# Optimization experiments

Measured on AMD Instinct MI355X. Metric: run time of the kernel, lower is better.

Reference implementation:

```python
import jax, jax.numpy as jnp
import numpy as np

N = 240000
B = 2
GRID = (480, 360, 32)
NUM_CLASS = 20
IGNORE_LABEL = 0
MINB = np.array([0.0, -np.pi, -4.0], np.float32)
MAXB = np.array([50.0, np.pi, 2.0], np.float32)
EPS = 1e-5


def setup_inputs() -> dict:
    key = jax.random.key(0)
    ks = jax.random.split(key, 32)
    d = {}
    d['pt_fea'] = jax.random.normal(ks[0], (N, 6), jnp.float32)
    # cylindrical coords (rho, phi, z) uniformly inside the volume
    u = jax.random.uniform(ks[1], (N, 3), jnp.float32)
    d['xyz'] = u * jnp.asarray(MAXB - MINB) + jnp.asarray(MINB)
    d['batch_idx'] = jnp.sort(jax.random.randint(ks[2], (N,), 0, B)).astype(jnp.int64)
    d['pt_lab'] = jax.random.randint(ks[3], (N,), 0, NUM_CLASS).astype(jnp.int64)
    d['shuffled_ind'] = jnp.arange(N, dtype=jnp.int64)  # identity perm (deterministic)
    i = 4
    for name, c in [('bn0', 9), ('bn1', 64), ('bn2', 128), ('bn3', 256)]:
        d[name + '_g'] = jax.random.uniform(ks[i], (c,), jnp.float32, 0.5, 1.5); i += 1
        d[name + '_b'] = jax.random.normal(ks[i], (c,), jnp.float32) * 0.1; i += 1
        d[name + '_m'] = jax.random.normal(ks[i], (c,), jnp.float32) * 0.1; i += 1
        d[name + '_v'] = jax.random.uniform(ks[i], (c,), jnp.float32, 0.5, 1.5); i += 1
    for name, (fi, fo) in [('1', (9, 64)), ('2', (64, 128)), ('3', (128, 256)), ('4', (256, 256))]:
        d['w' + name] = jax.random.normal(ks[i], (fi, fo), jnp.float32) / np.sqrt(fi); i += 1
        d['b' + name] = jax.random.normal(ks[i], (fo,), jnp.float32) * 0.01; i += 1
    d['wc'] = jax.random.normal(ks[i], (256, 16), jnp.float32) / 16.0; i += 1
    d['bc'] = jax.random.normal(ks[i], (16,), jnp.float32) * 0.01
    return d


def _bn(x, g, b, m, v):
    return (x - m) * (g * jax.lax.rsqrt(v + EPS)) + b


def _ppmodel(feat, bn0_g, bn0_b, bn0_m, bn0_v, w1, b1, bn1_g, bn1_b, bn1_m, bn1_v,
             w2, b2, bn2_g, bn2_b, bn2_m, bn2_v, w3, b3, bn3_g, bn3_b, bn3_m, bn3_v, w4, b4):
    x = _bn(feat, bn0_g, bn0_b, bn0_m, bn0_v)
    x = jax.nn.relu(_bn(x @ w1 + b1, bn1_g, bn1_b, bn1_m, bn1_v))
    x = jax.nn.relu(_bn(x @ w2 + b2, bn2_g, bn2_b, bn2_m, bn2_v))
    x = jax.nn.relu(_bn(x @ w3 + b3, bn3_g, bn3_b, bn3_m, bn3_v))
    return x @ w4 + b4  # [N, 256]


def reference(pt_fea, xyz, batch_idx, pt_lab, shuffled_ind,
              bn0_g, bn0_b, bn0_m, bn0_v, w1, b1, bn1_g, bn1_b, bn1_m, bn1_v,
              w2, b2, bn2_g, bn2_b, bn2_m, bn2_v, w3, b3, bn3_g, bn3_b, bn3_m, bn3_v,
              w4, b4, wc, bc):
    minb = jnp.asarray(MINB)
    maxb = jnp.asarray(MAXB)
    grid = jnp.asarray(np.array(GRID, np.float32))
    intervals = (maxb - minb) / (grid - 1.0)

    clamped = jnp.clip(xyz, minb, maxb)
    ind = jnp.floor((clamped - minb) / intervals).astype(jnp.int32)  # [N,3]
    voxel_centers = (ind.astype(jnp.float32) + 0.5) * intervals + minb
    rel_xyz = xyz - voxel_centers
    feat = jnp.concatenate([rel_xyz, pt_fea], axis=1)  # [N,9]

    bi = batch_idx.astype(jnp.int32)
    counts = jnp.full((B,) + GRID + (NUM_CLASS,), IGNORE_LABEL, jnp.int32)
    counts = counts.at[bi, ind[:, 0], ind[:, 1], ind[:, 2], pt_lab].add(1)
    voxel_labels = jnp.argmax(counts, axis=-1).astype(jnp.int32)  # [B,480,360,32]

    feat = feat[shuffled_ind]

    flat = ((bi.astype(jnp.int64) * GRID[0] + ind[:, 0]) * GRID[1] + ind[:, 1]) * GRID[2] + ind[:, 2]
    unq, unq_inv = jnp.unique(flat, size=N, fill_value=-1, return_inverse=True)
    unq_inv = unq_inv.reshape(-1)

    processed = _ppmodel(feat, bn0_g, bn0_b, bn0_m, bn0_v, w1, b1, bn1_g, bn1_b, bn1_m, bn1_v,
                         w2, b2, bn2_g, bn2_b, bn2_m, bn2_v, w3, b3, bn3_g, bn3_b, bn3_m, bn3_v, w4, b4)
    pooled = jax.ops.segment_max(processed, unq_inv, num_segments=N)
    seg_cnt = jax.ops.segment_sum(jnp.ones((N,), jnp.float32), unq_inv, num_segments=N)
    pooled = jnp.where(seg_cnt[:, None] > 0, pooled, 0.0)  # zero out empty (padded) segments

    processed_pooled = jax.nn.relu(pooled @ wc + bc)  # fea_compression

    cat_pt_ind = jnp.concatenate([batch_idx[:, None], ind.astype(jnp.int64)], axis=1)
    return (unq, processed_pooled, voxel_labels, cat_pt_ind)
```

## Files before the change

kernel.cpp:

```cpp
#include <hip/hip_runtime.h>
#include <stdint.h>

#define N_PTS 240000
#define NV    11059200
#define NWORDS 172800
#define NB_PT 938
#define NB_WORD 675
#define NBLK_MLP 3750
#define PA 264

typedef __bf16 bf16x8 __attribute__((ext_vector_type(8)));
typedef short  short8 __attribute__((ext_vector_type(8)));
typedef float  f32x4  __attribute__((ext_vector_type(4)));

__device__ __forceinline__ unsigned short f2bf(float f) {
  unsigned u = __builtin_bit_cast(unsigned, f);
  return (unsigned short)((u + 0x7FFFu + ((u >> 16) & 1u)) >> 16);
}
__device__ __forceinline__ float bf2f(unsigned short h) {
  unsigned u = ((unsigned)h) << 16;
  return __builtin_bit_cast(float, u);
}

__device__ __forceinline__ unsigned block_sum(unsigned v, unsigned* s4, int t) {
  #pragma unroll
  for (int o = 32; o; o >>= 1) v += __shfl_down(v, o);
  if ((t & 63) == 0) s4[t >> 6] = v;
  __syncthreads();
  unsigned r = s4[0] + s4[1] + s4[2] + s4[3];
  __syncthreads();
  return r;
}

__global__ void prep_vox_kernel(
    const float* __restrict__ bng0, const float* __restrict__ bnb0, const float* __restrict__ bnm0, const float* __restrict__ bnv0,
    const float* __restrict__ bng1, const float* __restrict__ bnb1, const float* __restrict__ bnm1, const float* __restrict__ bnv1,
    const float* __restrict__ bng2, const float* __restrict__ bnb2, const float* __restrict__ bnm2, const float* __restrict__ bnv2,
    const float* __restrict__ bng3, const float* __restrict__ bnb3, const float* __restrict__ bnm3, const float* __restrict__ bnv3,
    const float* __restrict__ w1, const float* __restrict__ b1,
    const float* __restrict__ w2, const float* __restrict__ b2,
    const float* __restrict__ w3, const float* __restrict__ b3,
    const float* __restrict__ w4, const float* __restrict__ wc,
    float* __restrict__ s0, float* __restrict__ t0, float* __restrict__ w1e, float* __restrict__ be1,
    float* __restrict__ be2, float* __restrict__ be3,
    unsigned short* __restrict__ w2t, unsigned short* __restrict__ w3t, unsigned short* __restrict__ w4t,
    unsigned short* __restrict__ wct,
    const float* __restrict__ xyz, const int* __restrict__ bidx,
    unsigned* __restrict__ flatkeys, unsigned long long* __restrict__ bitmap,
    float* __restrict__ out_cat, float* __restrict__ out_unq)
{
  if (blockIdx.x < 256) {
    const int id = blockIdx.x * 256 + threadIdx.x;
    { int c = id >> 8, k = id & 255; w4t[c * 256 + k] = f2bf(w4[k * 256 + c]); }
    if (id < 32768) { int c = id >> 7, k = id & 127;
      float s = bng3[c] * rsqrtf(bnv3[c] + 1e-5f);
      w3t[c * 128 + k] = f2bf(w3[k * 256 + c] * s); }
    if (id < 8192) { int c = id >> 6, k = id & 63;
      float s = bng2[c] * rsqrtf(bnv2[c] + 1e-5f);
      w2t[c * 64 + k] = f2bf(w2[k * 128 + c] * s); }
    if (id < 4096) { int c = id >> 8, k = id & 255;
      wct[c * 256 + k] = f2bf(wc[k * 16 + c]); }
    if (id < 576) { int k = id / 64, c = id % 64;
      float s = bng1[c] * rsqrtf(bnv1[c] + 1e-5f);
      w1e[k * 64 + c] = w1[k * 64 + c] * s; }
    if (id < 64)  { float s = bng1[id] * rsqrtf(bnv1[id] + 1e-5f); be1[id] = (b1[id] - bnm1[id]) * s + bnb1[id]; }
    if (id < 128) { float s = bng2[id] * rsqrtf(bnv2[id] + 1e-5f); be2[id] = (b2[id] - bnm2[id]) * s + bnb2[id]; }
    if (id < 256) { float s = bng3[id] * rsqrtf(bnv3[id] + 1e-5f); be3[id] = (b3[id] - bnm3[id]) * s + bnb3[id]; }
    if (id < 9)   { float s = bng0[id] * rsqrtf(bnv0[id] + 1e-5f); s0[id] = s; t0[id] = bnb0[id] - bnm0[id] * s; }
    return;
  }
  const int j = (blockIdx.x - 256) * 256 + threadIdx.x;
  if (j >= N_PTS) return;
  out_unq[j] = -1.0f;
  const float PI_F = 3.14159265358979323846f;
  const float minb[3] = {0.0f, -PI_F, -4.0f};
  const float maxb[3] = {50.0f, PI_F, 2.0f};
  const float gm1[3]  = {479.0f, 359.0f, 31.0f};
  int ind[3];
  #pragma unroll
  for (int d = 0; d < 3; ++d) {
    float itv = (maxb[d] - minb[d]) / gm1[d];
    float x  = xyz[(size_t)j * 3 + d];
    float cl = fminf(fmaxf(x, minb[d]), maxb[d]);
    ind[d] = (int)floorf((cl - minb[d]) / itv);
  }
  const int bi = bidx[j];
  const unsigned flat = ((unsigned)(bi * 480 + ind[0]) * 360u + (unsigned)ind[1]) * 32u + (unsigned)ind[2];
  flatkeys[j] = flat;
  atomicOr(&bitmap[flat >> 6], 1ull << (flat & 63u));
  float* oc = out_cat + (size_t)j * 4;
  oc[0] = (float)bi; oc[1] = (float)ind[0]; oc[2] = (float)ind[1]; oc[3] = (float)ind[2];
}

__global__ void reduce_words(const unsigned long long* __restrict__ bm, unsigned* __restrict__ bsums) {
  __shared__ unsigned sh[256];
  const int w = blockIdx.x * 256 + threadIdx.x;
  sh[threadIdx.x] = (unsigned)__popcll(bm[w]);
  __syncthreads();
  for (int s = 128; s > 0; s >>= 1) { if (threadIdx.x < s) sh[threadIdx.x] += sh[threadIdx.x + s]; __syncthreads(); }
  if (threadIdx.x == 0) bsums[blockIdx.x] = sh[0];
}

__global__ __launch_bounds__(256) void scatter_unq(
    const unsigned long long* __restrict__ bm, const unsigned* __restrict__ bsums,
    unsigned* __restrict__ wordpref, unsigned* __restrict__ unqvals, float* __restrict__ out_unq)
{
  __shared__ unsigned sh[256];
  __shared__ unsigned s4[4];
  const int t = threadIdx.x, b = blockIdx.x;
  const int w = b * 256 + t;
  unsigned long long word = bm[w];
  unsigned own = (unsigned)__popcll(word);
  sh[t] = own; __syncthreads();
  for (int off = 1; off < 256; off <<= 1) {
    unsigned v = (t >= off) ? sh[t - off] : 0u;
    __syncthreads(); sh[t] += v; __syncthreads();
  }
  unsigned v = 0;
  for (int i = t; i < b; i += 256) v += bsums[i];
  const unsigned excl = block_sum(v, s4, t);
  unsigned r = excl + sh[t] - own;
  wordpref[w] = r;
  while (word) {
    int bit = __builtin_ctzll(word);
    unsigned id = (unsigned)w * 64u + (unsigned)bit;
    unqvals[r] = id;
    out_unq[r] = (float)id;
    ++r;
    word &= word - 1;
  }
}

__global__ void inv_kernel(const unsigned* __restrict__ flatkeys, const unsigned long long* __restrict__ bm,
                           const unsigned* __restrict__ wordpref,
                           unsigned* __restrict__ unq_inv, unsigned* __restrict__ cnt) {
  const int j = blockIdx.x * 256 + threadIdx.x;
  if (j >= N_PTS) return;
  const unsigned f = flatkeys[j];
  const unsigned w = f >> 6, b = f & 63u;
  const unsigned r = wordpref[w] + (unsigned)__popcll(bm[w] & ((1ull << b) - 1ull));
  unq_inv[j] = r;
  atomicAdd(&cnt[r], 1u);
}

__global__ void reduce_cnt(const unsigned* __restrict__ cnt, unsigned* __restrict__ bsums) {
  __shared__ unsigned sh[256];
  const int j = blockIdx.x * 256 + threadIdx.x;
  sh[threadIdx.x] = (j < N_PTS) ? cnt[j] : 0u;
  __syncthreads();
  for (int s = 128; s > 0; s >>= 1) { if (threadIdx.x < s) sh[threadIdx.x] += sh[threadIdx.x + s]; __syncthreads(); }
  if (threadIdx.x == 0) bsums[blockIdx.x] = sh[0];
}

__global__ __launch_bounds__(256) void scan_cnt(
    const unsigned* __restrict__ cnt, const unsigned* __restrict__ bsums,
    unsigned* __restrict__ off, unsigned* __restrict__ cur)
{
  __shared__ unsigned sh[256];
  __shared__ unsigned s4[4];
  const int t = threadIdx.x, b = blockIdx.x;
  const int j = b * 256 + t;
  unsigned own = (j < N_PTS) ? cnt[j] : 0u;
  sh[t] = own; __syncthreads();
  for (int o = 1; o < 256; o <<= 1) {
    unsigned v = (t >= o) ? sh[t - o] : 0u;
    __syncthreads(); sh[t] += v; __syncthreads();
  }
  unsigned v = 0;
  for (int i = t; i < b; i += 256) v += bsums[i];
  const unsigned excl = block_sum(v, s4, t);
  if (j < N_PTS) { unsigned e = excl + sh[t] - own; off[j] = e; cur[j] = e; }
}

__global__ void plist_fill_kernel(const unsigned* __restrict__ unq_inv, unsigned* __restrict__ cur,
                                  unsigned long long* __restrict__ plist64,
                                  const unsigned* __restrict__ cnt, const float* __restrict__ bc,
                                  float* __restrict__ out_pooled) {
  const int j = blockIdx.x * 256 + threadIdx.x;
  if (j >= N_PTS) return;
  const unsigned r = unq_inv[j];
  plist64[atomicAdd(&cur[r], 1u)] = ((unsigned long long)r << 32) | (unsigned)j;
  if (cnt[j] == 0) {
    #pragma unroll
    for (int c = 0; c < 16; ++c) out_pooled[(size_t)j * 16 + c] = fmaxf(bc[c], 0.f);
  }
}

template<int K, int C, bool RELU, bool MIDB>
__device__ __forceinline__ void gemm_stage(
    const unsigned short* __restrict__ Wt,
    const float* __restrict__ bias,
    const unsigned short* in,
    unsigned short* outp,
    int wave, int l15, int quad)
{
  constexpr int KC = K / 32;
  constexpr int NT = C / 64;
  f32x4 acc[4][NT];
  #pragma unroll
  for (int mt = 0; mt < 4; ++mt)
    #pragma unroll
    for (int nt = 0; nt < NT; ++nt) acc[mt][nt] = (f32x4){0.f, 0.f, 0.f, 0.f};
  const unsigned short* wp[NT];
  #pragma unroll
  for (int nt = 0; nt < NT; ++nt)
    wp[nt] = Wt + (size_t)(wave * 16 * NT + nt * 16 + l15) * K + quad * 8;
  bf16x8 b0[NT], b1r[NT], b2r[NT];
  #pragma unroll
  for (int nt = 0; nt < NT; ++nt)
    b0[nt] = __builtin_bit_cast(bf16x8, *(const short8*)(wp[nt]));
  if (KC > 1) {
    #pragma unroll
    for (int nt = 0; nt < NT; ++nt)
      b1r[nt] = __builtin_bit_cast(bf16x8, *(const short8*)(wp[nt] + 32));
  }
  #pragma unroll
  for (int kc = 0; kc < KC; ++kc) {
    if (kc + 2 < KC) {
      #pragma unroll
      for (int nt = 0; nt < NT; ++nt)
        b2r[nt] = __builtin_bit_cast(bf16x8, *(const short8*)(wp[nt] + (kc + 2) * 32));
    }
    __builtin_amdgcn_s_setprio(1);
    #pragma unroll
    for (int mt = 0; mt < 4; ++mt) {
      bf16x8 a = __builtin_bit_cast(bf16x8, *(const short8*)&in[(mt * 16 + l15) * PA + kc * 32 + quad * 8]);
      #pragma unroll
      for (int nt = 0; nt < NT; ++nt)
        acc[mt][nt] = __builtin_amdgcn_mfma_f32_16x16x32_bf16(b0[nt], a, acc[mt][nt], 0, 0, 0);
    }
    __builtin_amdgcn_s_setprio(0);
    #pragma unroll
    for (int nt = 0; nt < NT; ++nt) { b0[nt] = b1r[nt]; b1r[nt] = b2r[nt]; }
  }
  if (MIDB) __syncthreads();
  #pragma unroll
  for (int mt = 0; mt < 4; ++mt)
    #pragma unroll
    for (int nt = 0; nt < NT; ++nt) {
      const int cbase = wave * 16 * NT + nt * 16 + quad * 4;
      const f32x4 bs = *(const f32x4*)&bias[cbase];
      unsigned short h[4];
      #pragma unroll
      for (int r = 0; r < 4; ++r) {
        float y = acc[mt][nt][r] + bs[r];
        if (RELU) y = fmaxf(y, 0.f);
        h[r] = f2bf(y);
      }
      uint2 pk; pk.x = (unsigned)h[0] | ((unsigned)h[1] << 16);
      pk.y = (unsigned)h[2] | ((unsigned)h[3] << 16);
      *(uint2*)&outp[(mt * 16 + l15) * PA + cbase] = pk;
    }
  __syncthreads();
}

__global__ __launch_bounds__(256, 3) void mlp_pool_kernel(
    const float* __restrict__ ptfea, const float* __restrict__ xyz, const int* __restrict__ shuf,
    const unsigned long long* __restrict__ plist64,
    const unsigned* __restrict__ offv, const unsigned* __restrict__ cnt,
    const int* __restrict__ ptlab, const unsigned* __restrict__ unqvals,
    const float* __restrict__ s0, const float* __restrict__ t0,
    const float* __restrict__ w1e, const float* __restrict__ be1,
    const unsigned short* __restrict__ w2t, const float* __restrict__ be2,
    const unsigned short* __restrict__ w3t, const float* __restrict__ be3,
    const unsigned short* __restrict__ w4t, const float* __restrict__ b4,
    const unsigned short* __restrict__ wct, const float* __restrict__ bc,
    unsigned short* __restrict__ partials, float* __restrict__ out_pooled,
    float* __restrict__ out_lab)
{
  __shared__ __align__(16) unsigned short buf[64 * PA];
  __shared__ int segs[64];
  __shared__ int jrows[64];
  __shared__ int s_alast;
  __shared__ int s_nrun;
  __shared__ unsigned short s_runs[32];
  __shared__ unsigned char s_lead[64], s_comp[64];
  const int tid  = threadIdx.x;
  const int wave = tid >> 6, lane = tid & 63;
  const int l15 = lane & 15, quad = lane >> 4;
  const int row0 = blockIdx.x * 64;

  if (tid == 0) { s_alast = 0; s_nrun = 0; }
  if (lane < 16) {
    const int r = wave * 16 + lane;
    const unsigned long long v = plist64[row0 + r];
    jrows[r] = (int)(unsigned)v;
    segs[r]  = (int)(unsigned)(v >> 32);
  }

  {
    const int r = wave * 16 + (lane >> 2), part = lane & 3;
    const int sj = shuf[jrows[r]];
    const float PI_F = 3.14159265358979323846f;
    const float minb[3] = {0.0f, -PI_F, -4.0f};
    const float maxb[3] = {50.0f, PI_F, 2.0f};
    const float gm1[3]  = {479.0f, 359.0f, 31.0f};
    float x0[9];
    #pragma unroll
    for (int d = 0; d < 3; ++d) {
      float itv = (maxb[d] - minb[d]) / gm1[d];
      float x   = xyz[(size_t)sj * 3 + d];
      float cl  = fminf(fmaxf(x, minb[d]), maxb[d]);
      float fi  = floorf((cl - minb[d]) / itv);
      float center = (fi + 0.5f) * itv + minb[d];
      x0[d] = (x - center) * s0[d] + t0[d];
    }
    #pragma unroll
    for (int d = 0; d < 6; ++d) x0[3 + d] = ptfea[(size_t)sj * 6 + d] * s0[3 + d] + t0[3 + d];
    unsigned short h[16];
    #pragma unroll
    for (int ci = 0; ci < 16; ++ci) {
      float acc = be1[part * 16 + ci];
      #pragma unroll
      for (int k = 0; k < 9; ++k) acc += x0[k] * w1e[k * 64 + part * 16 + ci];
      h[ci] = f2bf(fmaxf(acc, 0.0f));
    }
    *(short8*)&buf[r * PA + part * 16]     = *(short8*)&h[0];
    *(short8*)&buf[r * PA + part * 16 + 8] = *(short8*)&h[8];
  }
  __syncthreads();

  if (tid < 64) {
    const int r = tid;
    bool lead = (r == 0) || (segs[r] != segs[r - 1]);
    s_lead[r] = lead ? 1 : 0;
    unsigned char comp = 0;
    int e = r + 1;
    if (lead) {
      atomicMax(&s_alast, r);
      while (e < 64 && segs[e] == segs[r]) ++e;
      const unsigned s = (unsigned)segs[r];
      comp = (offv[s] == (unsigned)(row0 + r) && offv[s] + cnt[s] == (unsigned)(row0 + e)) ? 1 : 0;
    }
    s_comp[r] = comp;
    if (comp) {
      int bestl;
      if (e - r == 1) bestl = ptlab[jrows[r]];
      else {
        int bestc = 0; bestl = 32;
        for (int i = r; i < e; ++i) {
          const int li = ptlab[jrows[i]];
          int cc = 0;
          for (int k2 = r; k2 < e; ++k2) cc += (ptlab[jrows[k2]] == li) ? 1 : 0;
          if (cc > bestc || (cc == bestc && li < bestl)) { bestc = cc; bestl = li; }
        }
      }
      out_lab[unqvals[segs[r]]] = (float)bestl;
    }
    const bool multi = lead && (e - r) > 1;
    unsigned long long mm = __ballot(multi);
    if (multi) {
      int idx = (int)__popcll(mm & ((1ull << r) - 1ull));
      s_runs[idx] = (unsigned short)((r << 8) | e);
    }
    if (tid == 0) s_nrun = (int)__popcll(mm);
  }

  gemm_stage< 64, 128, true,  false>(w2t, be2, buf,       buf + 136, wave, l15, quad);
  gemm_stage<128, 256, true,  true >(w3t, be3, buf + 136, buf,       wave, l15, quad);
  gemm_stage<256, 256, false, true >(w4t, b4,  buf,       buf,       wave, l15, quad);

  {
    const int n = s_nrun;
    for (int i = 0; i < n; ++i) {
      const int re = s_runs[i];
      const int r = re >> 8, e = re & 255;
      float m = bf2f(buf[r * PA + tid]);
      for (int rr = r + 1; rr < e; ++rr) m = fmaxf(m, bf2f(buf[rr * PA + tid]));
      buf[r * PA + tid] = f2bf(m);
    }
  }
  __syncthreads();

  {
    const int c = tid;
    const int alast = s_alast;
    const size_t b2 = (size_t)blockIdx.x * 2;
    if (!s_comp[0])     partials[b2 * 256 + c]       = buf[0 * PA + c];
    if (!s_comp[alast]) partials[(b2 + 1) * 256 + c] = buf[alast * PA + c];
  }

  {
    const unsigned short* wp = wct + l15 * 256 + quad * 8;
    bf16x8 wv[8];
    #pragma unroll
    for (int kc = 0; kc < 8; ++kc)
      wv[kc] = __builtin_bit_cast(bf16x8, *(const short8*)(wp + kc * 32));
    f32x4 acc = (f32x4){0.f, 0.f, 0.f, 0.f};
    #pragma unroll
    for (int kc = 0; kc < 8; ++kc) {
      bf16x8 x = __builtin_bit_cast(bf16x8, *(const short8*)&buf[(wave * 16 + l15) * PA + kc * 32 + quad * 8]);
      acc = __builtin_amdgcn_mfma_f32_16x16x32_bf16(wv[kc], x, acc, 0, 0, 0);
    }
    const int r1 = wave * 16 + l15;
    if (s_lead[r1] && s_comp[r1]) {
      const f32x4 bcv = *(const f32x4*)&bc[quad * 4];
      f32x4 v;
      #pragma unroll
      for (int r = 0; r < 4; ++r) v[r] = fmaxf(acc[r] + bcv[r], 0.f);
      *(f32x4*)&out_pooled[(size_t)segs[r1] * 16 + quad * 4] = v;
    }
  }
}

__global__ __launch_bounds__(256) void merge_kernel(
    const unsigned long long* __restrict__ plist64,
    const unsigned* __restrict__ offv, const unsigned* __restrict__ cnt,
    const unsigned short* __restrict__ partials,
    const int* __restrict__ ptlab, const unsigned* __restrict__ unqvals,
    const float* __restrict__ wc, const float* __restrict__ bc,
    float* __restrict__ out_pooled, float* __restrict__ out_lab)
{
  __shared__ float pooled[256];
  __shared__ float psum[256];
  const int b = blockIdx.x;
  const unsigned s = (unsigned)(plist64[(size_t)b * 64 + 63] >> 32);
  const unsigned o = offv[s], e = o + cnt[s];
  if ((o >> 6) != (unsigned)b) return;
  if (e <= (unsigned)(b + 1) * 64) return;
  const int B1 = (int)((e - 1) >> 6);
  const int c = threadIdx.x;
  float m = bf2f(partials[((size_t)2 * b + 1) * 256 + c]);
  for (int bb = b + 1; bb <= B1; ++bb)
    m = fmaxf(m, bf2f(partials[(size_t)2 * bb * 256 + c]));
  pooled[c] = m;
  __syncthreads();
  const int co = c & 15, kg = c >> 4;
  float p = 0.f;
  #pragma unroll
  for (int k = kg * 16; k < kg * 16 + 16; ++k) p += pooled[k] * wc[k * 16 + co];
  psum[c] = p;
  __syncthreads();
  if (c < 16) {
    float acc = bc[c];
    #pragma unroll
    for (int g = 0; g < 16; ++g) acc += psum[g * 16 + c];
    out_pooled[(size_t)s * 16 + c] = fmaxf(acc, 0.f);
  }
  if (c == 0) {
    int bestc = 0, bestl = 32;
    for (unsigned i = o; i < e; ++i) {
      const int li = ptlab[(unsigned)plist64[i]];
      int cc = 0;
      for (unsigned k2 = o; k2 < e; ++k2) cc += (ptlab[(unsigned)plist64[k2]] == li) ? 1 : 0;
      if (cc > bestc || (cc == bestc && li < bestl)) { bestc = cc; bestl = li; }
    }
    out_lab[unqvals[s]] = (float)bestl;
  }
}

extern "C" void kernel_launch(void* const* d_in, const int* in_sizes, int n_in,
                              void* d_out, int out_size, void* d_ws, size_t ws_size,
                              hipStream_t stream)
{
  const float* pt_fea = (const float*)d_in[0];
  const float* xyz    = (const float*)d_in[1];
  const int*   bidx   = (const int*)d_in[2];
  const int*   ptlab  = (const int*)d_in[3];
  const int*   shuf   = (const int*)d_in[4];
  const float* bng0 = (const float*)d_in[5],  *bnb0 = (const float*)d_in[6],  *bnm0 = (const float*)d_in[7],  *bnv0 = (const float*)d_in[8];
  const float* bng1 = (const float*)d_in[9],  *bnb1 = (const float*)d_in[10], *bnm1 = (const float*)d_in[11], *bnv1 = (const float*)d_in[12];
  const float* bng2 = (const float*)d_in[13], *bnb2 = (const float*)d_in[14], *bnm2 = (const float*)d_in[15], *bnv2 = (const float*)d_in[16];
  const float* bng3 = (const float*)d_in[17], *bnb3 = (const float*)d_in[18], *bnm3 = (const float*)d_in[19], *bnv3 = (const float*)d_in[20];
  const float* w1 = (const float*)d_in[21], *b1 = (const float*)d_in[22];
  const float* w2 = (const float*)d_in[23], *b2 = (const float*)d_in[24];
  const float* w3 = (const float*)d_in[25], *b3 = (const float*)d_in[26];
  const float* w4 = (const float*)d_in[27], *b4 = (const float*)d_in[28];
  const float* wc = (const float*)d_in[29], *bc = (const float*)d_in[30];

  float* out        = (float*)d_out;
  float* out_unq    = out;
  float* out_pooled = out + 240000;
  float* out_lab    = out + 4080000;
  float* out_cat    = out + 15139200;

  char* wsb = (char*)d_ws;
  size_t o = 0;
  auto alloc = [&](size_t bytes) -> void* { void* p = wsb + o; o = (o + bytes + 255) & ~(size_t)255; return p; };
  unsigned long long* bitmap = (unsigned long long*)alloc((size_t)NWORDS * 8);
  unsigned* cnt    = (unsigned*)alloc((size_t)N_PTS * 4);
  const size_t zero_bytes = o;
  float* s0  = (float*)alloc(9 * 4);
  float* t0  = (float*)alloc(9 * 4);
  float* w1e = (float*)alloc(576 * 4);
  float* be1 = (float*)alloc(64 * 4);
  float* be2 = (float*)alloc(128 * 4);
  float* be3 = (float*)alloc(256 * 4);
  unsigned short* w2t = (unsigned short*)alloc(8192 * 2);
  unsigned short* w3t = (unsigned short*)alloc(32768 * 2);
  unsigned short* w4t = (unsigned short*)alloc(65536 * 2);
  unsigned short* wct = (unsigned short*)alloc(4096 * 2);
  unsigned* flatkeys = (unsigned*)alloc((size_t)N_PTS * 4);
  unsigned* unq_inv  = (unsigned*)alloc((size_t)N_PTS * 4);
  unsigned* unqvals  = (unsigned*)alloc((size_t)N_PTS * 4);
  unsigned* offv     = (unsigned*)alloc((size_t)N_PTS * 4);
  unsigned* cur      = (unsigned*)alloc((size_t)N_PTS * 4);
  unsigned long long* plist64 = (unsigned long long*)alloc((size_t)N_PTS * 8);
  unsigned* wordpref = (unsigned*)alloc((size_t)NWORDS * 4);
  unsigned* bsumA    = (unsigned*)alloc(NB_WORD * 4);
  unsigned* bsumB    = (unsigned*)alloc(NB_PT * 4);
  unsigned short* partials = (unsigned short*)alloc((size_t)NBLK_MLP * 2 * 256 * 2);

  hipMemsetAsync(bitmap, 0, zero_bytes, stream);
  hipMemsetAsync(out_lab, 0, (size_t)NV * 4, stream);

  prep_vox_kernel<<<256 + NB_PT, 256, 0, stream>>>(
      bng0, bnb0, bnm0, bnv0, bng1, bnb1, bnm1, bnv1,
      bng2, bnb2, bnm2, bnv2, bng3, bnb3, bnm3, bnv3,
      w1, b1, w2, b2, w3, b3, w4, wc,
      s0, t0, w1e, be1, be2, be3, w2t, w3t, w4t, wct,
      xyz, bidx, flatkeys, bitmap, out_cat, out_unq);
  reduce_words<<<NB_WORD, 256, 0, stream>>>(bitmap, bsumA);
  scatter_unq<<<NB_WORD, 256, 0, stream>>>(bitmap, bsumA, wordpref, unqvals, out_unq);
  inv_kernel<<<NB_PT, 256, 0, stream>>>(flatkeys, bitmap, wordpref, unq_inv, cnt);
  reduce_cnt<<<NB_PT, 256, 0, stream>>>(cnt, bsumB);
  scan_cnt<<<NB_PT, 256, 0, stream>>>(cnt, bsumB, offv, cur);
  plist_fill_kernel<<<NB_PT, 256, 0, stream>>>(unq_inv, cur, plist64, cnt, bc, out_pooled);
  mlp_pool_kernel<<<NBLK_MLP, 256, 0, stream>>>(pt_fea, xyz, shuf, plist64, offv, cnt,
                                                ptlab, unqvals,
                                                s0, t0, w1e, be1, w2t, be2, w3t, be3, w4t, b4,
                                                wct, bc, partials, out_pooled, out_lab);
  merge_kernel<<<NBLK_MLP, 256, 0, stream>>>(plist64, offv, cnt, partials,
                                             ptlab, unqvals, wc, bc, out_pooled, out_lab);
}
```

Measured before the change: 352.8 us.

## Fuse seven voxelization/scan kernels into one persistent kernel with grid barriers

```diff
diff --git a/kernel.cpp b/kernel.cpp
--- a/kernel.cpp
+++ b/kernel.cpp
@@ -7,6 +7,8 @@
 #define NB_PT 938
 #define NB_WORD 675
 #define NBLK_MLP 3750
+#define NBLK_MID 768
+#define NVB_P0  1194
 #define PA 264
 
 typedef __bf16 bf16x8 __attribute__((ext_vector_type(8)));
@@ -32,7 +34,24 @@
   return r;
 }
 
-__global__ void prep_vox_kernel(
+__device__ __forceinline__ void gbar(unsigned* bar) {
+  __threadfence();
+  __syncthreads();
+  if (threadIdx.x == 0) {
+    unsigned g = __hip_atomic_load(&bar[1], __ATOMIC_ACQUIRE, __HIP_MEMORY_SCOPE_AGENT);
+    unsigned a = __hip_atomic_fetch_add(&bar[0], 1u, __ATOMIC_ACQ_REL, __HIP_MEMORY_SCOPE_AGENT);
+    if (a + 1u == (unsigned)NBLK_MID) {
+      __hip_atomic_store(&bar[0], 0u, __ATOMIC_RELAXED, __HIP_MEMORY_SCOPE_AGENT);
+      __hip_atomic_fetch_add(&bar[1], 1u, __ATOMIC_RELEASE, __HIP_MEMORY_SCOPE_AGENT);
+    } else {
+      while (__hip_atomic_load(&bar[1], __ATOMIC_ACQUIRE, __HIP_MEMORY_SCOPE_AGENT) == g)
+        __builtin_amdgcn_s_sleep(8);
+    }
+  }
+  __syncthreads();
+}
+
+__global__ __launch_bounds__(256, 4) void fused_mid_kernel(
     const float* __restrict__ bng0, const float* __restrict__ bnb0, const float* __restrict__ bnm0, const float* __restrict__ bnv0,
     const float* __restrict__ bng1, const float* __restrict__ bnb1, const float* __restrict__ bnm1, const float* __restrict__ bnv1,
     const float* __restrict__ bng2, const float* __restrict__ bnb2, const float* __restrict__ bnm2, const float* __restrict__ bnv2,
@@ -47,142 +66,147 @@
     unsigned short* __restrict__ wct,
     const float* __restrict__ xyz, const int* __restrict__ bidx,
     unsigned* __restrict__ flatkeys, unsigned long long* __restrict__ bitmap,
-    float* __restrict__ out_cat, float* __restrict__ out_unq)
-{
-  if (blockIdx.x < 256) {
-    const int id = blockIdx.x * 256 + threadIdx.x;
-    { int c = id >> 8, k = id & 255; w4t[c * 256 + k] = f2bf(w4[k * 256 + c]); }
-    if (id < 32768) { int c = id >> 7, k = id & 127;
-      float s = bng3[c] * rsqrtf(bnv3[c] + 1e-5f);
-      w3t[c * 128 + k] = f2bf(w3[k * 256 + c] * s); }
-    if (id < 8192) { int c = id >> 6, k = id & 63;
-      float s = bng2[c] * rsqrtf(bnv2[c] + 1e-5f);
-      w2t[c * 64 + k] = f2bf(w2[k * 128 + c] * s); }
-    if (id < 4096) { int c = id >> 8, k = id & 255;
-      wct[c * 256 + k] = f2bf(wc[k * 16 + c]); }
-    if (id < 576) { int k = id / 64, c = id % 64;
-      float s = bng1[c] * rsqrtf(bnv1[c] + 1e-5f);
-      w1e[k * 64 + c] = w1[k * 64 + c] * s; }
-    if (id < 64)  { float s = bng1[id] * rsqrtf(bnv1[id] + 1e-5f); be1[id] = (b1[id] - bnm1[id]) * s + bnb1[id]; }
-    if (id < 128) { float s = bng2[id] * rsqrtf(bnv2[id] + 1e-5f); be2[id] = (b2[id] - bnm2[id]) * s + bnb2[id]; }
-    if (id < 256) { float s = bng3[id] * rsqrtf(bnv3[id] + 1e-5f); be3[id] = (b3[id] - bnm3[id]) * s + bnb3[id]; }
-    if (id < 9)   { float s = bng0[id] * rsqrtf(bnv0[id] + 1e-5f); s0[id] = s; t0[id] = bnb0[id] - bnm0[id] * s; }
-    return;
-  }
-  const int j = (blockIdx.x - 256) * 256 + threadIdx.x;
-  if (j >= N_PTS) return;
-  out_unq[j] = -1.0f;
-  const float PI_F = 3.14159265358979323846f;
-  const float minb[3] = {0.0f, -PI_F, -4.0f};
-  const float maxb[3] = {50.0f, PI_F, 2.0f};
-  const float gm1[3]  = {479.0f, 359.0f, 31.0f};
-  int ind[3];
-  #pragma unroll
-  for (int d = 0; d < 3; ++d) {
-    float itv = (maxb[d] - minb[d]) / gm1[d];
-    float x  = xyz[(size_t)j * 3 + d];
-    float cl = fminf(fmaxf(x, minb[d]), maxb[d]);
-    ind[d] = (int)floorf((cl - minb[d]) / itv);
-  }
-  const int bi = bidx[j];
-  const unsigned flat = ((unsigned)(bi * 480 + ind[0]) * 360u + (unsigned)ind[1]) * 32u + (unsigned)ind[2];
-  flatkeys[j] = flat;
-  atomicOr(&bitmap[flat >> 6], 1ull << (flat & 63u));
-  float* oc = out_cat + (size_t)j * 4;
-  oc[0] = (float)bi; oc[1] = (float)ind[0]; oc[2] = (float)ind[1]; oc[3] = (float)ind[2];
-}
-
-__global__ void reduce_words(const unsigned long long* __restrict__ bm, unsigned* __restrict__ bsums) {
-  __shared__ unsigned sh[256];
-  const int w = blockIdx.x * 256 + threadIdx.x;
-  sh[threadIdx.x] = (unsigned)__popcll(bm[w]);
-  __syncthreads();
-  for (int s = 128; s > 0; s >>= 1) { if (threadIdx.x < s) sh[threadIdx.x] += sh[threadIdx.x + s]; __syncthreads(); }
-  if (threadIdx.x == 0) bsums[blockIdx.x] = sh[0];
-}
-
-__global__ __launch_bounds__(256) void scatter_unq(
-    const unsigned long long* __restrict__ bm, const unsigned* __restrict__ bsums,
-    unsigned* __restrict__ wordpref, unsigned* __restrict__ unqvals, float* __restrict__ out_unq)
+    float* __restrict__ out_cat, float* __restrict__ out_unq,
+    unsigned* __restrict__ bsumA, unsigned* __restrict__ wordpref, unsigned* __restrict__ unqvals,
+    unsigned* __restrict__ unq_inv, unsigned* __restrict__ cnt,
+    unsigned* __restrict__ bsumB, unsigned* __restrict__ offv, unsigned* __restrict__ cur,
+    unsigned long long* __restrict__ plist64, const float* __restrict__ bc,
+    float* __restrict__ out_pooled, unsigned* __restrict__ bar)
 {
   __shared__ unsigned sh[256];
   __shared__ unsigned s4[4];
-  const int t = threadIdx.x, b = blockIdx.x;
-  const int w = b * 256 + t;
-  unsigned long long word = bm[w];
-  unsigned own = (unsigned)__popcll(word);
-  sh[t] = own; __syncthreads();
-  for (int off = 1; off < 256; off <<= 1) {
-    unsigned v = (t >= off) ? sh[t - off] : 0u;
-    __syncthreads(); sh[t] += v; __syncthreads();
-  }
-  unsigned v = 0;
-  for (int i = t; i < b; i += 256) v += bsums[i];
-  const unsigned excl = block_sum(v, s4, t);
-  unsigned r = excl + sh[t] - own;
-  wordpref[w] = r;
-  while (word) {
-    int bit = __builtin_ctzll(word);
-    unsigned id = (unsigned)w * 64u + (unsigned)bit;
-    unqvals[r] = id;
-    out_unq[r] = (float)id;
-    ++r;
-    word &= word - 1;
-  }
-}
-
-__global__ void inv_kernel(const unsigned* __restrict__ flatkeys, const unsigned long long* __restrict__ bm,
-                           const unsigned* __restrict__ wordpref,
-                           unsigned* __restrict__ unq_inv, unsigned* __restrict__ cnt) {
-  const int j = blockIdx.x * 256 + threadIdx.x;
-  if (j >= N_PTS) return;
-  const unsigned f = flatkeys[j];
-  const unsigned w = f >> 6, b = f & 63u;
-  const unsigned r = wordpref[w] + (unsigned)__popcll(bm[w] & ((1ull << b) - 1ull));
-  unq_inv[j] = r;
-  atomicAdd(&cnt[r], 1u);
-}
-
-__global__ void reduce_cnt(const unsigned* __restrict__ cnt, unsigned* __restrict__ bsums) {
-  __shared__ unsigned sh[256];
-  const int j = blockIdx.x * 256 + threadIdx.x;
-  sh[threadIdx.x] = (j < N_PTS) ? cnt[j] : 0u;
-  __syncthreads();
-  for (int s = 128; s > 0; s >>= 1) { if (threadIdx.x < s) sh[threadIdx.x] += sh[threadIdx.x + s]; __syncthreads(); }
-  if (threadIdx.x == 0) bsums[blockIdx.x] = sh[0];
-}
-
-__global__ __launch_bounds__(256) void scan_cnt(
-    const unsigned* __restrict__ cnt, const unsigned* __restrict__ bsums,
-    unsigned* __restrict__ off, unsigned* __restrict__ cur)
-{
-  __shared__ unsigned sh[256];
-  __shared__ unsigned s4[4];
-  const int t = threadIdx.x, b = blockIdx.x;
-  const int j = b * 256 + t;
-  unsigned own = (j < N_PTS) ? cnt[j] : 0u;
-  sh[t] = own; __syncthreads();
-  for (int o = 1; o < 256; o <<= 1) {
-    unsigned v = (t >= o) ? sh[t - o] : 0u;
-    __syncthreads(); sh[t] += v; __syncthreads();
-  }
-  unsigned v = 0;
-  for (int i = t; i < b; i += 256) v += bsums[i];
-  const unsigned excl = block_sum(v, s4, t);
-  if (j < N_PTS) { unsigned e = excl + sh[t] - own; off[j] = e; cur[j] = e; }
-}
-
-__global__ void plist_fill_kernel(const unsigned* __restrict__ unq_inv, unsigned* __restrict__ cur,
-                                  unsigned long long* __restrict__ plist64,
-                                  const unsigned* __restrict__ cnt, const float* __restrict__ bc,
-                                  float* __restrict__ out_pooled) {
-  const int j = blockIdx.x * 256 + threadIdx.x;
-  if (j >= N_PTS) return;
-  const unsigned r = unq_inv[j];
-  plist64[atomicAdd(&cur[r], 1u)] = ((unsigned long long)r << 32) | (unsigned)j;
-  if (cnt[j] == 0) {
-    #pragma unroll
-    for (int c = 0; c < 16; ++c) out_pooled[(size_t)j * 16 + c] = fmaxf(bc[c], 0.f);
+  const int t = threadIdx.x;
+
+  for (int vb = blockIdx.x; vb < NVB_P0; vb += NBLK_MID) {
+    if (vb < 256) {
+      const int id = vb * 256 + t;
+      { int c = id >> 8, k = id & 255; w4t[c * 256 + k] = f2bf(w4[k * 256 + c]); }
+      if (id < 32768) { int c = id >> 7, k = id & 127;
+        float s = bng3[c] * rsqrtf(bnv3[c] + 1e-5f);
+        w3t[c * 128 + k] = f2bf(w3[k * 256 + c] * s); }
+      if (id < 8192) { int c = id >> 6, k = id & 63;
+        float s = bng2[c] * rsqrtf(bnv2[c] + 1e-5f);
+        w2t[c * 64 + k] = f2bf(w2[k * 128 + c] * s); }
+      if (id < 4096) { int c = id >> 8, k = id & 255;
+        wct[c * 256 + k] = f2bf(wc[k * 16 + c]); }
+      if (id < 576) { int k = id / 64, c = id % 64;
+        float s = bng1[c] * rsqrtf(bnv1[c] + 1e-5f);
+        w1e[k * 64 + c] = w1[k * 64 + c] * s; }
+      if (id < 64)  { float s = bng1[id] * rsqrtf(bnv1[id] + 1e-5f); be1[id] = (b1[id] - bnm1[id]) * s + bnb1[id]; }
+      if (id < 128) { float s = bng2[id] * rsqrtf(bnv2[id] + 1e-5f); be2[id] = (b2[id] - bnm2[id]) * s + bnb2[id]; }
+      if (id < 256) { float s = bng3[id] * rsqrtf(bnv3[id] + 1e-5f); be3[id] = (b3[id] - bnm3[id]) * s + bnb3[id]; }
+      if (id < 9)   { float s = bng0[id] * rsqrtf(bnv0[id] + 1e-5f); s0[id] = s; t0[id] = bnb0[id] - bnm0[id] * s; }
+    } else {
+      const int j = (vb - 256) * 256 + t;
+      if (j < N_PTS) {
+        out_unq[j] = -1.0f;
+        const float PI_F = 3.14159265358979323846f;
+        const float minb[3] = {0.0f, -PI_F, -4.0f};
+        const float maxb[3] = {50.0f, PI_F, 2.0f};
+        const float gm1[3]  = {479.0f, 359.0f, 31.0f};
+        int ind[3];
+        #pragma unroll
+        for (int d = 0; d < 3; ++d) {
+          float itv = (maxb[d] - minb[d]) / gm1[d];
+          float x  = xyz[(size_t)j * 3 + d];
+          float cl = fminf(fmaxf(x, minb[d]), maxb[d]);
+          ind[d] = (int)floorf((cl - minb[d]) / itv);
+        }
+        const int bi = bidx[j];
+        const unsigned flat = ((unsigned)(bi * 480 + ind[0]) * 360u + (unsigned)ind[1]) * 32u + (unsigned)ind[2];
+        flatkeys[j] = flat;
+        atomicOr(&bitmap[flat >> 6], 1ull << (flat & 63u));
+        float* oc = out_cat + (size_t)j * 4;
+        oc[0] = (float)bi; oc[1] = (float)ind[0]; oc[2] = (float)ind[1]; oc[3] = (float)ind[2];
+      }
+    }
+  }
+  gbar(bar);
+
+  for (int vb = blockIdx.x; vb < NB_WORD; vb += NBLK_MID) {
+    const int w = vb * 256 + t;
+    sh[t] = (unsigned)__popcll(bitmap[w]);
+    __syncthreads();
+    for (int s = 128; s > 0; s >>= 1) { if (t < s) sh[t] += sh[t + s]; __syncthreads(); }
+    if (t == 0) bsumA[vb] = sh[0];
+    __syncthreads();
+  }
+  gbar(bar);
+
+  for (int vb = blockIdx.x; vb < NB_WORD; vb += NBLK_MID) {
+    const int w = vb * 256 + t;
+    unsigned long long word = bitmap[w];
+    unsigned own = (unsigned)__popcll(word);
+    sh[t] = own; __syncthreads();
+    for (int off = 1; off < 256; off <<= 1) {
+      unsigned v = (t >= off) ? sh[t - off] : 0u;
+      __syncthreads(); sh[t] += v; __syncthreads();
+    }
+    unsigned v = 0;
+    for (int i = t; i < vb; i += 256) v += bsumA[i];
+    const unsigned excl = block_sum(v, s4, t);
+    unsigned r = excl + sh[t] - own;
+    wordpref[w] = r;
+    while (word) {
+      int bit = __builtin_ctzll(word);
+      unsigned id = (unsigned)w * 64u + (unsigned)bit;
+      unqvals[r] = id;
+      out_unq[r] = (float)id;
+      ++r;
+      word &= word - 1;
+    }
+    __syncthreads();
+  }
+  gbar(bar);
+
+  for (int vb = blockIdx.x; vb < NB_PT; vb += NBLK_MID) {
+    const int j = vb * 256 + t;
+    if (j < N_PTS) {
+      const unsigned f = flatkeys[j];
+      const unsigned w = f >> 6, b = f & 63u;
+      const unsigned r = wordpref[w] + (unsigned)__popcll(bitmap[w] & ((1ull << b) - 1ull));
+      unq_inv[j] = r;
+      atomicAdd(&cnt[r], 1u);
+    }
+  }
+  gbar(bar);
+
+  for (int vb = blockIdx.x; vb < NB_PT; vb += NBLK_MID) {
+    const int j = vb * 256 + t;
+    sh[t] = (j < N_PTS) ? cnt[j] : 0u;
+    __syncthreads();
+    for (int s = 128; s > 0; s >>= 1) { if (t < s) sh[t] += sh[t + s]; __syncthreads(); }
+    if (t == 0) bsumB[vb] = sh[0];
+    __syncthreads();
+  }
+  gbar(bar);
+
+  for (int vb = blockIdx.x; vb < NB_PT; vb += NBLK_MID) {
+    const int j = vb * 256 + t;
+    unsigned own = (j < N_PTS) ? cnt[j] : 0u;
+    sh[t] = own; __syncthreads();
+    for (int o = 1; o < 256; o <<= 1) {
+      unsigned v = (t >= o) ? sh[t - o] : 0u;
+      __syncthreads(); sh[t] += v; __syncthreads();
+    }
+    unsigned v = 0;
+    for (int i = t; i < vb; i += 256) v += bsumB[i];
+    const unsigned excl = block_sum(v, s4, t);
+    if (j < N_PTS) { unsigned e = excl + sh[t] - own; offv[j] = e; cur[j] = e; }
+    __syncthreads();
+  }
+  gbar(bar);
+
+  for (int vb = blockIdx.x; vb < NB_PT; vb += NBLK_MID) {
+    const int j = vb * 256 + t;
+    if (j < N_PTS) {
+      const unsigned r = unq_inv[j];
+      plist64[atomicAdd(&cur[r], 1u)] = ((unsigned long long)r << 32) | (unsigned)j;
+      if (cnt[j] == 0) {
+        #pragma unroll
+        for (int c = 0; c < 16; ++c) out_pooled[(size_t)j * 16 + c] = fmaxf(bc[c], 0.f);
+      }
+    }
   }
 }
 
@@ -479,6 +503,7 @@
   auto alloc = [&](size_t bytes) -> void* { void* p = wsb + o; o = (o + bytes + 255) & ~(size_t)255; return p; };
   unsigned long long* bitmap = (unsigned long long*)alloc((size_t)NWORDS * 8);
   unsigned* cnt    = (unsigned*)alloc((size_t)N_PTS * 4);
+  unsigned* bar    = (unsigned*)alloc(2 * 4);
   const size_t zero_bytes = o;
   float* s0  = (float*)alloc(9 * 4);
   float* t0  = (float*)alloc(9 * 4);
@@ -504,18 +529,14 @@
   hipMemsetAsync(bitmap, 0, zero_bytes, stream);
   hipMemsetAsync(out_lab, 0, (size_t)NV * 4, stream);
 
-  prep_vox_kernel<<<256 + NB_PT, 256, 0, stream>>>(
+  fused_mid_kernel<<<NBLK_MID, 256, 0, stream>>>(
       bng0, bnb0, bnm0, bnv0, bng1, bnb1, bnm1, bnv1,
       bng2, bnb2, bnm2, bnv2, bng3, bnb3, bnm3, bnv3,
       w1, b1, w2, b2, w3, b3, w4, wc,
       s0, t0, w1e, be1, be2, be3, w2t, w3t, w4t, wct,
-      xyz, bidx, flatkeys, bitmap, out_cat, out_unq);
-  reduce_words<<<NB_WORD, 256, 0, stream>>>(bitmap, bsumA);
-  scatter_unq<<<NB_WORD, 256, 0, stream>>>(bitmap, bsumA, wordpref, unqvals, out_unq);
-  inv_kernel<<<NB_PT, 256, 0, stream>>>(flatkeys, bitmap, wordpref, unq_inv, cnt);
-  reduce_cnt<<<NB_PT, 256, 0, stream>>>(cnt, bsumB);
-  scan_cnt<<<NB_PT, 256, 0, stream>>>(cnt, bsumB, offv, cur);
-  plist_fill_kernel<<<NB_PT, 256, 0, stream>>>(unq_inv, cur, plist64, cnt, bc, out_pooled);
+      xyz, bidx, flatkeys, bitmap, out_cat, out_unq,
+      bsumA, wordpref, unqvals, unq_inv, cnt, bsumB, offv, cur,
+      plist64, bc, out_pooled, bar);
   mlp_pool_kernel<<<NBLK_MLP, 256, 0, stream>>>(pt_fea, xyz, shuf, plist64, offv, cnt,
                                                 ptlab, unqvals,
                                                 s0, t0, w1e, be1, w2t, be2, w3t, be3, w4t, b4,
```

After: 1.147 ms. 225% more time.

## Make MLP-pool kernel persistent over six tiles with software-prefetched point data

Applied to the files above, without the earlier changes.

```diff
diff --git a/kernel.cpp b/kernel.cpp
--- a/kernel.cpp
+++ b/kernel.cpp
@@ -7,6 +7,8 @@
 #define NB_PT 938
 #define NB_WORD 675
 #define NBLK_MLP 3750
+#define NPERS 625
+#define TILES 6
 #define PA 264
 
 typedef __bf16 bf16x8 __attribute__((ext_vector_type(8)));
@@ -269,137 +271,176 @@
     float* __restrict__ out_lab)
 {
   __shared__ __align__(16) unsigned short buf[64 * PA];
-  __shared__ int segs[64];
-  __shared__ int jrows[64];
-  __shared__ int s_alast;
-  __shared__ int s_nrun;
-  __shared__ unsigned short s_runs[32];
-  __shared__ unsigned char s_lead[64], s_comp[64];
+  __shared__ int segs[2][64];
+  __shared__ int jrows[2][64];
+  __shared__ int s_alast[2];
+  __shared__ int s_nrun[2];
+  __shared__ unsigned short s_runs[2][32];
+  __shared__ unsigned char s_lead[2][64], s_comp[2][64];
   const int tid  = threadIdx.x;
   const int wave = tid >> 6, lane = tid & 63;
   const int l15 = lane & 15, quad = lane >> 4;
-  const int row0 = blockIdx.x * 64;
-
-  if (tid == 0) { s_alast = 0; s_nrun = 0; }
-  if (lane < 16) {
-    const int r = wave * 16 + lane;
-    const unsigned long long v = plist64[row0 + r];
-    jrows[r] = (int)(unsigned)v;
-    segs[r]  = (int)(unsigned)(v >> 32);
-  }
-
+  const int gr   = wave * 16 + (lane >> 2);
+  const int part = lane & 3;
+
+  const float PI_F = 3.14159265358979323846f;
+  const float minb[3] = {0.0f, -PI_F, -4.0f};
+  const float maxb[3] = {50.0f, PI_F, 2.0f};
+  const float gm1[3]  = {479.0f, 359.0f, 31.0f};
+
+  int jr, sg, sj;
+  float xz[3], fe[6];
   {
-    const int r = wave * 16 + (lane >> 2), part = lane & 3;
-    const int sj = shuf[jrows[r]];
-    const float PI_F = 3.14159265358979323846f;
-    const float minb[3] = {0.0f, -PI_F, -4.0f};
-    const float maxb[3] = {50.0f, PI_F, 2.0f};
-    const float gm1[3]  = {479.0f, 359.0f, 31.0f};
-    float x0[9];
-    #pragma unroll
-    for (int d = 0; d < 3; ++d) {
-      float itv = (maxb[d] - minb[d]) / gm1[d];
-      float x   = xyz[(size_t)sj * 3 + d];
-      float cl  = fminf(fmaxf(x, minb[d]), maxb[d]);
-      float fi  = floorf((cl - minb[d]) / itv);
-      float center = (fi + 0.5f) * itv + minb[d];
-      x0[d] = (x - center) * s0[d] + t0[d];
-    }
-    #pragma unroll
-    for (int d = 0; d < 6; ++d) x0[3 + d] = ptfea[(size_t)sj * 6 + d] * s0[3 + d] + t0[3 + d];
-    unsigned short h[16];
-    #pragma unroll
-    for (int ci = 0; ci < 16; ++ci) {
-      float acc = be1[part * 16 + ci];
-      #pragma unroll
-      for (int k = 0; k < 9; ++k) acc += x0[k] * w1e[k * 64 + part * 16 + ci];
-      h[ci] = f2bf(fmaxf(acc, 0.0f));
-    }
-    *(short8*)&buf[r * PA + part * 16]     = *(short8*)&h[0];
-    *(short8*)&buf[r * PA + part * 16 + 8] = *(short8*)&h[8];
-  }
-  __syncthreads();
-
-  if (tid < 64) {
-    const int r = tid;
-    bool lead = (r == 0) || (segs[r] != segs[r - 1]);
-    s_lead[r] = lead ? 1 : 0;
-    unsigned char comp = 0;
-    int e = r + 1;
-    if (lead) {
-      atomicMax(&s_alast, r);
-      while (e < 64 && segs[e] == segs[r]) ++e;
-      const unsigned s = (unsigned)segs[r];
-      comp = (offv[s] == (unsigned)(row0 + r) && offv[s] + cnt[s] == (unsigned)(row0 + e)) ? 1 : 0;
-    }
-    s_comp[r] = comp;
-    if (comp) {
-      int bestl;
-      if (e - r == 1) bestl = ptlab[jrows[r]];
-      else {
-        int bestc = 0; bestl = 32;
-        for (int i = r; i < e; ++i) {
-          const int li = ptlab[jrows[i]];
-          int cc = 0;
-          for (int k2 = r; k2 < e; ++k2) cc += (ptlab[jrows[k2]] == li) ? 1 : 0;
-          if (cc > bestc || (cc == bestc && li < bestl)) { bestc = cc; bestl = li; }
+    const unsigned long long v = plist64[(size_t)blockIdx.x * TILES * 64 + gr];
+    jr = (int)(unsigned)v; sg = (int)(unsigned)(v >> 32);
+    sj = shuf[jr];
+    #pragma unroll
+    for (int d = 0; d < 3; ++d) xz[d] = xyz[(size_t)sj * 3 + d];
+    #pragma unroll
+    for (int d = 0; d < 6; ++d) fe[d] = ptfea[(size_t)sj * 6 + d];
+  }
+
+  for (int tile = 0; tile < TILES; ++tile) {
+    const int btile = blockIdx.x * TILES + tile;
+    const int row0  = btile * 64;
+    const int pb    = tile & 1;
+    const bool hn   = (tile + 1 < TILES);
+
+    if (tid == 0) { s_alast[pb] = 0; s_nrun[pb] = 0; }
+    if (part == 0) { jrows[pb][gr] = jr; segs[pb][gr] = sg; }
+
+    {
+      float x0[9];
+      #pragma unroll
+      for (int d = 0; d < 3; ++d) {
+        float itv = (maxb[d] - minb[d]) / gm1[d];
+        float cl  = fminf(fmaxf(xz[d], minb[d]), maxb[d]);
+        float fi  = floorf((cl - minb[d]) / itv);
+        float center = (fi + 0.5f) * itv + minb[d];
+        x0[d] = (xz[d] - center) * s0[d] + t0[d];
+      }
+      #pragma unroll
+      for (int d = 0; d < 6; ++d) x0[3 + d] = fe[d] * s0[3 + d] + t0[3 + d];
+      unsigned short h[16];
+      #pragma unroll
+      for (int ci = 0; ci < 16; ++ci) {
+        float acc = be1[part * 16 + ci];
+        #pragma unroll
+        for (int k = 0; k < 9; ++k) acc += x0[k] * w1e[k * 64 + part * 16 + ci];
+        h[ci] = f2bf(fmaxf(acc, 0.0f));
+      }
+      *(short8*)&buf[gr * PA + part * 16]     = *(short8*)&h[0];
+      *(short8*)&buf[gr * PA + part * 16 + 8] = *(short8*)&h[8];
+    }
+    __syncthreads();
+
+    unsigned long long vn = 0;
+    if (hn) vn = plist64[(size_t)row0 + 64 + gr];
+
+    if (tid < 64) {
+      const int r = tid;
+      bool lead = (r == 0) || (segs[pb][r] != segs[pb][r - 1]);
+      s_lead[pb][r] = lead ? 1 : 0;
+      unsigned char comp = 0;
+      int e = r + 1;
+      if (lead) {
+        atomicMax(&s_alast[pb], r);
+        while (e < 64 && segs[pb][e] == segs[pb][r]) ++e;
+        const unsigned s = (unsigned)segs[pb][r];
+        comp = (offv[s] == (unsigned)(row0 + r) && offv[s] + cnt[s] == (unsigned)(row0 + e)) ? 1 : 0;
+      }
+      s_comp[pb][r] = comp;
+      if (comp) {
+        int bestl;
+        if (e - r == 1) bestl = ptlab[jrows[pb][r]];
+        else {
+          int bestc = 0; bestl = 32;
+          for (int i = r; i < e; ++i) {
+            const int li = ptlab[jrows[pb][i]];
+            int cc = 0;
+            for (int k2 = r; k2 < e; ++k2) cc += (ptlab[jrows[pb][k2]] == li) ? 1 : 0;
+            if (cc > bestc || (cc == bestc && li < bestl)) { bestc = cc; bestl = li; }
+          }
         }
-      }
-      out_lab[unqvals[segs[r]]] = (float)bestl;
-    }
-    const bool multi = lead && (e - r) > 1;
-    unsigned long long mm = __ballot(multi);
-    if (multi) {
-      int idx = (int)__popcll(mm & ((1ull << r) - 1ull));
-      s_runs[idx] = (unsigned short)((r << 8) | e);
-    }
-    if (tid == 0) s_nrun = (int)__popcll(mm);
-  }
-
-  gemm_stage< 64, 128, true,  false>(w2t, be2, buf,       buf + 136, wave, l15, quad);
-  gemm_stage<128, 256, true,  true >(w3t, be3, buf + 136, buf,       wave, l15, quad);
-  gemm_stage<256, 256, false, true >(w4t, b4,  buf,       buf,       wave, l15, quad);
-
-  {
-    const int n = s_nrun;
-    for (int i = 0; i < n; ++i) {
-      const int re = s_runs[i];
-      const int r = re >> 8, e = re & 255;
-      float m = bf2f(buf[r * PA + tid]);
-      for (int rr = r + 1; rr < e; ++rr) m = fmaxf(m, bf2f(buf[rr * PA + tid]));
-      buf[r * PA + tid] = f2bf(m);
-    }
-  }
-  __syncthreads();
-
-  {
-    const int c = tid;
-    const int alast = s_alast;
-    const size_t b2 = (size_t)blockIdx.x * 2;
-    if (!s_comp[0])     partials[b2 * 256 + c]       = buf[0 * PA + c];
-    if (!s_comp[alast]) partials[(b2 + 1) * 256 + c] = buf[alast * PA + c];
-  }
-
-  {
-    const unsigned short* wp = wct + l15 * 256 + quad * 8;
-    bf16x8 wv[8];
-    #pragma unroll
-    for (int kc = 0; kc < 8; ++kc)
-      wv[kc] = __builtin_bit_cast(bf16x8, *(const short8*)(wp + kc * 32));
-    f32x4 acc = (f32x4){0.f, 0.f, 0.f, 0.f};
-    #pragma unroll
-    for (int kc = 0; kc < 8; ++kc) {
-      bf16x8 x = __builtin_bit_cast(bf16x8, *(const short8*)&buf[(wave * 16 + l15) * PA + kc * 32 + quad * 8]);
-      acc = __builtin_amdgcn_mfma_f32_16x16x32_bf16(wv[kc], x, acc, 0, 0, 0);
-    }
-    const int r1 = wave * 16 + l15;
-    if (s_lead[r1] && s_comp[r1]) {
-      const f32x4 bcv = *(const f32x4*)&bc[quad * 4];
-      f32x4 v;
-      #pragma unroll
-      for (int r = 0; r < 4; ++r) v[r] = fmaxf(acc[r] + bcv[r], 0.f);
-      *(f32x4*)&out_pooled[(size_t)segs[r1] * 16 + quad * 4] = v;
-    }
+        out_lab[unqvals[segs[pb][r]]] = (float)bestl;
+      }
+      const bool multi = lead && (e - r) > 1;
+      unsigned long long mm = __ballot(multi);
+      if (multi) {
+        int idx = (int)__popcll(mm & ((1ull << r) - 1ull));
+        s_runs[pb][idx] = (unsigned short)((r << 8) | e);
+      }
+      if (tid == 0) s_nrun[pb] = (int)__popcll(mm);
+    }
+
+    gemm_stage< 64, 128, true,  false>(w2t, be2, buf,       buf + 136, wave, l15, quad);
+
+    int jrn = 0, sgn = 0, sjn = 0;
+    if (hn) {
+      jrn = (int)(unsigned)vn; sgn = (int)(unsigned)(vn >> 32);
+      sjn = shuf[jrn];
+    }
+
+    gemm_stage<128, 256, true,  true >(w3t, be3, buf + 136, buf,       wave, l15, quad);
+
+    float xzn[3] = {0.f, 0.f, 0.f}, fen[6] = {0.f, 0.f, 0.f, 0.f, 0.f, 0.f};
+    if (hn) {
+      #pragma unroll
+      for (int d = 0; d < 3; ++d) xzn[d] = xyz[(size_t)sjn * 3 + d];
+      #pragma unroll
+      for (int d = 0; d < 6; ++d) fen[d] = ptfea[(size_t)sjn * 6 + d];
+    }
+
+    gemm_stage<256, 256, false, true >(w4t, b4,  buf,       buf,       wave, l15, quad);
+
+    {
+      const int n = s_nrun[pb];
+      for (int i = 0; i < n; ++i) {
+        const int re = s_runs[pb][i];
+        const int r = re >> 8, e = re & 255;
+        float m = bf2f(buf[r * PA + tid]);
+        for (int rr = r + 1; rr < e; ++rr) m = fmaxf(m, bf2f(buf[rr * PA + tid]));
+        buf[r * PA + tid] = f2bf(m);
+      }
+    }
+    __syncthreads();
+
+    {
+      const int c = tid;
+      const int alast = s_alast[pb];
+      const size_t b2 = (size_t)btile * 2;
+      if (!s_comp[pb][0])     partials[b2 * 256 + c]       = buf[0 * PA + c];
+      if (!s_comp[pb][alast]) partials[(b2 + 1) * 256 + c] = buf[alast * PA + c];
+    }
+
+    {
+      const unsigned short* wp = wct + l15 * 256 + quad * 8;
+      bf16x8 wv[8];
+      #pragma unroll
+      for (int kc = 0; kc < 8; ++kc)
+        wv[kc] = __builtin_bit_cast(bf16x8, *(const short8*)(wp + kc * 32));
+      f32x4 acc = (f32x4){0.f, 0.f, 0.f, 0.f};
+      #pragma unroll
+      for (int kc = 0; kc < 8; ++kc) {
+        bf16x8 x = __builtin_bit_cast(bf16x8, *(const short8*)&buf[(wave * 16 + l15) * PA + kc * 32 + quad * 8]);
+        acc = __builtin_amdgcn_mfma_f32_16x16x32_bf16(wv[kc], x, acc, 0, 0, 0);
+      }
+      const int r1 = wave * 16 + l15;
+      if (s_lead[pb][r1] && s_comp[pb][r1]) {
+        const f32x4 bcv = *(const f32x4*)&bc[quad * 4];
+        f32x4 v;
+        #pragma unroll
+        for (int r = 0; r < 4; ++r) v[r] = fmaxf(acc[r] + bcv[r], 0.f);
+        *(f32x4*)&out_pooled[(size_t)segs[pb][r1] * 16 + quad * 4] = v;
+      }
+    }
+
+    jr = jrn; sg = sgn; sj = sjn;
+    #pragma unroll
+    for (int d = 0; d < 3; ++d) xz[d] = xzn[d];
+    #pragma unroll
+    for (int d = 0; d < 6; ++d) fe[d] = fen[d];
+    __syncthreads();
   }
 }
 
@@ -516,10 +557,10 @@
   reduce_cnt<<<NB_PT, 256, 0, stream>>>(cnt, bsumB);
   scan_cnt<<<NB_PT, 256, 0, stream>>>(cnt, bsumB, offv, cur);
   plist_fill_kernel<<<NB_PT, 256, 0, stream>>>(unq_inv, cur, plist64, cnt, bc, out_pooled);
-  mlp_pool_kernel<<<NBLK_MLP, 256, 0, stream>>>(pt_fea, xyz, shuf, plist64, offv, cnt,
-                                                ptlab, unqvals,
-                                                s0, t0, w1e, be1, w2t, be2, w3t, be3, w4t, b4,
-                                                wct, bc, partials, out_pooled, out_lab);
+  mlp_pool_kernel<<<NPERS, 256, 0, stream>>>(pt_fea, xyz, shuf, plist64, offv, cnt,
+                                             ptlab, unqvals,
+                                             s0, t0, w1e, be1, w2t, be2, w3t, be3, w4t, b4,
+                                             wct, bc, partials, out_pooled, out_lab);
   merge_kernel<<<NBLK_MLP, 256, 0, stream>>>(plist64, offv, cnt, partials,
                                              ptlab, unqvals, wc, bc, out_pooled, out_lab);
 }
```

Result: slower. 679.5 us (+92.6%).
